# Kernel optimization log

Hardware: AMD Instinct MI355X
Metric: run time of the kernel (lower is better)

Reference implementation:

```python
import jax, jax.numpy as jnp
import numpy as np

DIM = 512
HEADS = 16
WS = 8          # window size
SHIFT = 4       # shift size
POSMLP = 32
MLP_HID = 4 * DIM
B = 32
HH = 56
WW = 56
EPS = 1e-5


def setup_inputs() -> dict:
    key = jax.random.key(0)
    ks = jax.random.split(key, 20)
    s = 0.02
    inp = {
        'x': jax.random.normal(ks[0], (B, HH * WW, DIM), jnp.float32),
        'g1': jnp.ones((DIM,), jnp.float32),
        'be1': jnp.zeros((DIM,), jnp.float32),
        'w_qkv': s * jax.random.normal(ks[1], (3 * DIM, DIM), jnp.float32),
        'b_qkv': jnp.zeros((3 * DIM,), jnp.float32),
        'pm_w1': s * jax.random.normal(ks[2], (POSMLP, 2), jnp.float32),
        'pm_b1': jnp.zeros((POSMLP,), jnp.float32),
        'pm_w2': s * jax.random.normal(ks[3], (HEADS, POSMLP), jnp.float32),
        'pm_b2': jnp.zeros((HEADS,), jnp.float32),
        'w_proj': s * jax.random.normal(ks[4], (DIM, DIM), jnp.float32),
        'b_proj': jnp.zeros((DIM,), jnp.float32),
        'g2': jnp.ones((DIM,), jnp.float32),
        'be2': jnp.zeros((DIM,), jnp.float32),
        'w_fc1': s * jax.random.normal(ks[5], (MLP_HID, DIM), jnp.float32),
        'b_fc1': jnp.zeros((MLP_HID,), jnp.float32),
        'w_fc2': s * jax.random.normal(ks[6], (DIM, MLP_HID), jnp.float32),
        'b_fc2': jnp.zeros((DIM,), jnp.float32),
        'H': HH,
        'W': WW,
    }
    return inp


def _layernorm(x, g, b):
    m = jnp.mean(x, -1, keepdims=True)
    v = jnp.mean(jnp.square(x - m), -1, keepdims=True)
    return (x - m) * jax.lax.rsqrt(v + EPS) * g + b


def _shift_mask(H, W, ws, sh):
    # static numpy construction of the (nW, N, N) 0/-100 shift mask
    img = np.zeros((H, W), np.float32)
    cnt = 0
    for hs in (slice(0, -ws), slice(-ws, -sh), slice(-sh, None)):
        for wsl in (slice(0, -ws), slice(-ws, -sh), slice(-sh, None)):
            img[hs, wsl] = cnt
            cnt += 1
    mw = img.reshape(H // ws, ws, W // ws, ws).transpose(0, 2, 1, 3).reshape(-1, ws * ws)
    diff = mw[:, None, :] - mw[:, :, None]
    return jnp.asarray(np.where(diff != 0, -100.0, 0.0).astype(np.float32))


def _pos_bias(ws, pm_w1, pm_b1, pm_w2, pm_b2):
    # log-CPB relative position bias computed by a tiny MLP -> (heads, N, N)
    g = jnp.stack(jnp.meshgrid(jnp.arange(ws), jnp.arange(ws), indexing='ij'))
    coords = g.reshape(2, -1).astype(jnp.float32)        # [2, N]
    d = coords[:, :, None] - coords[:, None, :]          # [2, N, N]
    d = jnp.sign(d) * jnp.log1p(jnp.abs(d))
    h = jax.nn.relu(jnp.einsum('cnm,oc->onm', d, pm_w1) + pm_b1[:, None, None])
    return jnp.einsum('onm,ho->hnm', h, pm_w2) + pm_b2[:, None, None]


def reference(x, g1, be1, w_qkv, b_qkv, pm_w1, pm_b1, pm_w2, pm_b2,
              w_proj, b_proj, g2, be2, w_fc1, b_fc1, w_fc2, b_fc2, H, W):
    ws, sh, nh = WS, SHIFT, HEADS
    Bb, L, C = x.shape
    hd = C // nh
    scale = hd ** -0.5
    N = ws * ws
    nWh, nWw = H // ws, W // ws
    nW = nWh * nWw

    shortcut = x
    xn = _layernorm(x, g1, be1).reshape(Bb, H, W, C)
    xn = jnp.roll(xn, (-sh, -sh), axis=(1, 2))
    # window partition -> (B*nW, N, C)
    xw = xn.reshape(Bb, nWh, ws, nWw, ws, C).transpose(0, 1, 3, 2, 4, 5).reshape(-1, N, C)

    qkv = (xw @ w_qkv.T + b_qkv).reshape(-1, N, 3, nh, hd).transpose(2, 0, 3, 1, 4)
    q, k, v = qkv[0], qkv[1], qkv[2]           # each (B*nW, nh, N, hd)

    attn = jnp.einsum('bhnd,bhmd->bhnm', q * scale, k)
    attn = attn + _pos_bias(ws, pm_w1, pm_b1, pm_w2, pm_b2)[None]

    mask = _shift_mask(H, W, ws, sh)           # (nW, N, N)
    attn = attn.reshape(Bb, nW, nh, N, N) + mask[None, :, None]
    attn = jax.nn.softmax(attn.reshape(-1, nh, N, N), axis=-1)

    out = jnp.einsum('bhnm,bhmd->bhnd', attn, v).transpose(0, 2, 1, 3).reshape(-1, N, C)
    out = out @ w_proj.T + b_proj

    # window reverse + roll back
    out = out.reshape(Bb, nWh, nWw, ws, ws, C).transpose(0, 1, 3, 2, 4, 5).reshape(Bb, H, W, C)
    out = jnp.roll(out, (sh, sh), axis=(1, 2)).reshape(Bb, L, C)

    x1 = shortcut + out
    h = jax.nn.gelu(_layernorm(x1, g2, be2) @ w_fc1.T + b_fc1, approximate=False)
    return x1 + (h @ w_fc2.T + b_fc2)
```

## Files before the change

### kernel.cpp

```cpp
#include <hip/hip_runtime.h>
#include <math.h>

typedef __bf16 bf16;
typedef bf16 bf16x8 __attribute__((ext_vector_type(8)));
typedef float f32x4 __attribute__((ext_vector_type(4)));

#define MFMA_BF16(a, b, c) __builtin_amdgcn_mfma_f32_16x16x32_bf16((a), (b), (c), 0, 0, 0)
#define GLDS16(gp, lp)                                                            \
  __builtin_amdgcn_global_load_lds((__attribute__((address_space(1))) void*)(gp), \
                                   (__attribute__((address_space(3))) void*)(lp), 16, 0, 0)

static constexpr int kDim   = 512;
static constexpr int kHeads = 16;
static constexpr int kHd    = 32;
static constexpr int kNt    = 64;
static constexpr int kNw    = 49;
static constexpr int kL     = 3136;
static constexpr int kToks  = 100352;
static constexpr int kWins  = 1568;
static constexpr int kHid   = 2048;
static constexpr size_t kQS = (size_t)kWins * kHeads * kNt * kHd;

__global__ __launch_bounds__(256) void wconv_kernel(const float* __restrict__ s,
                                                    bf16* __restrict__ d, int n8) {
  int i = blockIdx.x * 256 + threadIdx.x;
  if (i >= n8) return;
  const float4 a = *(const float4*)(s + i * 8);
  const float4 b = *(const float4*)(s + i * 8 + 4);
  bf16x8 o;
  o[0] = (bf16)a.x; o[1] = (bf16)a.y; o[2] = (bf16)a.z; o[3] = (bf16)a.w;
  o[4] = (bf16)b.x; o[5] = (bf16)b.y; o[6] = (bf16)b.z; o[7] = (bf16)b.w;
  *(bf16x8*)(d + i * 8) = o;
}

__global__ void posbias_kernel(const float* __restrict__ w1, const float* __restrict__ b1,
                               const float* __restrict__ w2, const float* __restrict__ b2,
                               float* __restrict__ tbl) {
  int idx = blockIdx.x * 256 + threadIdx.x;
  if (idx >= kHeads * kNt * kNt) return;
  int h = idx >> 12, n = (idx >> 6) & 63, m = idx & 63;
  float dr = (float)((n >> 3) - (m >> 3));
  float dc = (float)((n & 7) - (m & 7));
  dr = (dr > 0.f ? 1.f : (dr < 0.f ? -1.f : 0.f)) * log1pf(fabsf(dr));
  dc = (dc > 0.f ? 1.f : (dc < 0.f ? -1.f : 0.f)) * log1pf(fabsf(dc));
  float acc = b2[h];
  for (int o = 0; o < 32; ++o) {
    float hv = w1[o * 2] * dr + w1[o * 2 + 1] * dc + b1[o];
    acc += w2[h * 32 + o] * fmaxf(hv, 0.f);
  }
  tbl[idx] = acc;
}

template <int MODE>
__global__ __launch_bounds__(256) void ln_kernel(const float* __restrict__ x,
                                                 const float* __restrict__ g,
                                                 const float* __restrict__ be,
                                                 bf16* __restrict__ o) {
  const int t = blockIdx.x * 4 + (threadIdx.x >> 6);
  const int lane = threadIdx.x & 63;
  size_t src;
  if (MODE == 0) {
    const int win = t >> 6, n = t & 63;
    const int b = win / kNw, wi = win % kNw;
    const int h0 = ((wi / 7) * 8 + (n >> 3) + 4) % 56;
    const int w0 = ((wi % 7) * 8 + (n & 7) + 4) % 56;
    src = ((size_t)b * kL + h0 * 56 + w0) * kDim;
  } else {
    src = (size_t)t * kDim;
  }
  const float4 a = *(const float4*)(x + src + lane * 8);
  const float4 bq = *(const float4*)(x + src + lane * 8 + 4);
  float xf[8] = {a.x, a.y, a.z, a.w, bq.x, bq.y, bq.z, bq.w};
  float s = 0.f, s2 = 0.f;
#pragma unroll
  for (int j = 0; j < 8; ++j) { s += xf[j]; s2 += xf[j] * xf[j]; }
#pragma unroll
  for (int off = 32; off > 0; off >>= 1) { s += __shfl_xor(s, off); s2 += __shfl_xor(s2, off); }
  const float mean = s * (1.f / 512.f);
  const float rstd = rsqrtf(s2 * (1.f / 512.f) - mean * mean + 1e-5f);
  const float4 ga = *(const float4*)(g + lane * 8);
  const float4 gb = *(const float4*)(g + lane * 8 + 4);
  const float4 ba = *(const float4*)(be + lane * 8);
  const float4 bb = *(const float4*)(be + lane * 8 + 4);
  const float gv[8] = {ga.x, ga.y, ga.z, ga.w, gb.x, gb.y, gb.z, gb.w};
  const float bv[8] = {ba.x, ba.y, ba.z, ba.w, bb.x, bb.y, bb.z, bb.w};
  bf16x8 ov;
#pragma unroll
  for (int j = 0; j < 8; ++j) ov[j] = (bf16)((xf[j] - mean) * rstd * gv[j] + bv[j]);
  *(bf16x8*)(o + (size_t)t * kDim + lane * 8) = ov;
}

template <int EPI>
__global__ __launch_bounds__(256) void gemm_bt(const bf16* __restrict__ A, const bf16* __restrict__ B,
                                               const float* __restrict__ bias, void* __restrict__ Cv,
                                               const float* __restrict__ extra, int N, int K) {
  __shared__ bf16 lA[128 * 64];
  __shared__ bf16 lB[128 * 64];
  const int nbn = N >> 7;
  const int bm = (int)blockIdx.x / nbn, bn = (int)blockIdx.x % nbn;
  const int tid = threadIdx.x;
  const int wave = tid >> 6, lane = tid & 63;
  const int wm = (wave >> 1) * 64, wn = (wave & 1) * 64;
  const int quad = lane >> 4, l16 = lane & 15;
  const int m7 = l16 & 7;
  f32x4 acc[4][4] = {};
  const int rloc = tid >> 3;
  const int csw = ((tid & 7) ^ (rloc & 7)) * 8;
  const bf16* pa = A + (size_t)(bm * 128 + rloc) * K + csw;
  const bf16* pb = B + (size_t)(bn * 128 + rloc) * K + csw;
  for (int kt = 0; kt < K; kt += 64) {
#pragma unroll
    for (int i = 0; i < 4; ++i) GLDS16(pa + (size_t)i * 32 * K + kt, lA + i * 2048 + tid * 8);
#pragma unroll
    for (int i = 0; i < 4; ++i) GLDS16(pb + (size_t)i * 32 * K + kt, lB + i * 2048 + tid * 8);
    __syncthreads();
#pragma unroll
    for (int kk = 0; kk < 2; ++kk) {
      const int pc = ((kk * 4 + quad) ^ m7) * 8;
      bf16x8 af[4], bfr[4];
#pragma unroll
      for (int mi = 0; mi < 4; ++mi)
        af[mi] = *(const bf16x8*)(lA + (wm + mi * 16 + l16) * 64 + pc);
#pragma unroll
      for (int ni = 0; ni < 4; ++ni)
        bfr[ni] = *(const bf16x8*)(lB + (wn + ni * 16 + l16) * 64 + pc);
#pragma unroll
      for (int mi = 0; mi < 4; ++mi)
#pragma unroll
        for (int ni = 0; ni < 4; ++ni) acc[mi][ni] = MFMA_BF16(af[mi], bfr[ni], acc[mi][ni]);
    }
    __syncthreads();
  }
  bf16* Cb = (bf16*)Cv;
  float* Cf = (float*)Cv;
#pragma unroll
  for (int mi = 0; mi < 4; ++mi) {
#pragma unroll
    for (int ni = 0; ni < 4; ++ni) {
      const int col = bn * 128 + wn + ni * 16 + l16;
      const float bb = bias[col];
#pragma unroll
      for (int r = 0; r < 4; ++r) {
        const int row = bm * 128 + wm + mi * 16 + quad * 4 + r;
        float val = acc[mi][ni][r] + bb;
        if constexpr (EPI == 1) {
          const int which = col >> 9, head = (col >> 5) & 15, d = col & 31;
          const int win = row >> 6, n = row & 63;
          Cb[(size_t)which * kQS + (((size_t)win * kHeads + head) * kNt + n) * kHd + d] = (bf16)val;
        } else if constexpr (EPI == 2) {
          val = 0.5f * val * (1.f + erff(val * 0.70710678118654752f));
          Cb[(size_t)row * N + col] = (bf16)val;
        } else if constexpr (EPI == 3) {
          Cf[(size_t)row * N + col] = val + extra[(size_t)row * N + col];
        } else {
          const int win = row >> 6, n = row & 63;
          const int b = win / kNw, wi = win % kNw;
          const int h0 = ((wi / 7) * 8 + (n >> 3) + 4) % 56;
          const int w0 = ((wi % 7) * 8 + (n & 7) + 4) % 56;
          const size_t dst = ((size_t)b * kL + h0 * 56 + w0) * kDim + col;
          Cf[dst] = val + extra[dst];
        }
      }
    }
  }
}

__device__ __forceinline__ int reg3(int x) { return x < 48 ? 0 : (x < 52 ? 1 : 2); }

__global__ __launch_bounds__(128) void attn_kernel(const bf16* __restrict__ qkv,
                                                   const float* __restrict__ ptbl,
                                                   bf16* __restrict__ out) {
  __shared__ float Sb[2][64 * 65];
  __shared__ float Rs[2][64];
  __shared__ bf16  Pb[2][64 * 72];
  __shared__ bf16  Vt[2][32 * 72];
  const int w = threadIdx.x >> 6, lane = threadIdx.x & 63;
  const int gwh = blockIdx.x * 2 + w;
  const int win = gwh >> 4, h = gwh & 15;
  const int quad = lane >> 4, l16 = lane & 15;
  const bf16* q = qkv + ((size_t)win * kHeads + h) * (kNt * kHd);
  const bf16* k = q + kQS;
  const bf16* v = q + 2 * kQS;

#pragma unroll
  for (int i = 0; i < 4; ++i) {
    const int row = i * 16 + (lane >> 2);
    const int d0 = (lane & 3) * 8;
    bf16x8 vv = *(const bf16x8*)(v + row * kHd + d0);
#pragma unroll
    for (int j = 0; j < 8; ++j) Vt[w][(d0 + j) * 72 + row] = vv[j];
  }

  bf16x8 qf[4], kf[4];
#pragma unroll
  for (int i = 0; i < 4; ++i) qf[i] = *(const bf16x8*)(q + (i * 16 + l16) * kHd + quad * 8);
#pragma unroll
  for (int j = 0; j < 4; ++j) kf[j] = *(const bf16x8*)(k + (j * 16 + l16) * kHd + quad * 8);
  f32x4 sa[4][4] = {};
#pragma unroll
  for (int i = 0; i < 4; ++i)
#pragma unroll
    for (int j = 0; j < 4; ++j) sa[i][j] = MFMA_BF16(qf[i], kf[j], sa[i][j]);

  const int wi = win % kNw;
  const int hb = (wi / 7) * 8, wb = (wi % 7) * 8;
  const float* bh = ptbl + h * 4096;
#pragma unroll
  for (int i = 0; i < 4; ++i) {
#pragma unroll
    for (int j = 0; j < 4; ++j) {
      const int ct = j * 16 + l16;
      const int crg = reg3(hb + (ct >> 3)) * 3 + reg3(wb + (ct & 7));
#pragma unroll
      for (int r = 0; r < 4; ++r) {
        const int rt = i * 16 + quad * 4 + r;
        const int rrg = reg3(hb + (rt >> 3)) * 3 + reg3(wb + (rt & 7));
        float sv = sa[i][j][r] * 0.17677669529663687f + bh[rt * 64 + ct];
        if (rrg != crg) sv -= 100.f;
        Sb[w][rt * 65 + ct] = sv;
      }
    }
  }
  __syncthreads();

  float mx = -1e30f;
  for (int i = 0; i < 64; ++i) mx = fmaxf(mx, Sb[w][lane * 65 + i]);
  float sum = 0.f;
  for (int i = 0; i < 64; ++i) {
    const float p = __expf(Sb[w][lane * 65 + i] - mx);
    sum += p;
    Pb[w][lane * 72 + i] = (bf16)p;
  }
  Rs[w][lane] = 1.f / sum;
  __syncthreads();

  f32x4 oa[4][2] = {};
#pragma unroll
  for (int kk = 0; kk < 2; ++kk) {
    bf16x8 pf[4], vf[2];
#pragma unroll
    for (int mi = 0; mi < 4; ++mi)
      pf[mi] = *(const bf16x8*)(&Pb[w][(mi * 16 + l16) * 72 + kk * 32 + quad * 8]);
#pragma unroll
    for (int nj = 0; nj < 2; ++nj)
      vf[nj] = *(const bf16x8*)(&Vt[w][(nj * 16 + l16) * 72 + kk * 32 + quad * 8]);
#pragma unroll
    for (int mi = 0; mi < 4; ++mi)
#pragma unroll
      for (int nj = 0; nj < 2; ++nj) oa[mi][nj] = MFMA_BF16(pf[mi], vf[nj], oa[mi][nj]);
  }
#pragma unroll
  for (int mi = 0; mi < 4; ++mi)
#pragma unroll
    for (int nj = 0; nj < 2; ++nj)
#pragma unroll
      for (int r = 0; r < 4; ++r) {
        const int row = mi * 16 + quad * 4 + r;
        const int col = nj * 16 + l16;
        out[((size_t)win * kNt + row) * kDim + h * kHd + col] = (bf16)(oa[mi][nj][r] * Rs[w][row]);
      }
}

extern "C" void kernel_launch(void* const* d_in, const int* in_sizes, int n_in,
                              void* d_out, int out_size, void* d_ws, size_t ws_size,
                              hipStream_t stream) {
  (void)in_sizes; (void)n_in; (void)out_size; (void)ws_size;
  const float* x      = (const float*)d_in[0];
  const float* g1     = (const float*)d_in[1];
  const float* be1    = (const float*)d_in[2];
  const float* w_qkv  = (const float*)d_in[3];
  const float* b_qkv  = (const float*)d_in[4];
  const float* pm_w1  = (const float*)d_in[5];
  const float* pm_b1  = (const float*)d_in[6];
  const float* pm_w2  = (const float*)d_in[7];
  const float* pm_b2  = (const float*)d_in[8];
  const float* w_proj = (const float*)d_in[9];
  const float* b_proj = (const float*)d_in[10];
  const float* g2     = (const float*)d_in[11];
  const float* be2    = (const float*)d_in[12];
  const float* w_fc1  = (const float*)d_in[13];
  const float* b_fc1  = (const float*)d_in[14];
  const float* w_fc2  = (const float*)d_in[15];
  const float* b_fc2  = (const float*)d_in[16];
  float* out = (float*)d_out;
  char* ws = (char*)d_ws;

  constexpr size_t OFF_WB   = 1u << 20;
  constexpr size_t OFF_XW   = OFF_WB + (8u << 20);
  constexpr size_t SZ_ACT   = (size_t)kToks * kDim * 2;
  constexpr size_t OFF_QKV  = OFF_XW + SZ_ACT;
  float* biastbl = (float*)ws;
  bf16* wqb = (bf16*)(ws + OFF_WB);
  bf16* wpb = wqb + 786432;
  bf16* w1b = wpb + 262144;
  bf16* w2b = w1b + 1048576;
  bf16* xw    = (bf16*)(ws + OFF_XW);
  bf16* attnb = xw;
  bf16* xn2   = xw;
  bf16* qkvb = (bf16*)(ws + OFF_QKV);
  float* x1  = (float*)(ws + OFF_QKV);
  bf16* hbuf = (bf16*)(ws + OFF_QKV + (size_t)kToks * kDim * 4);

  wconv_kernel<<<dim3(786432 / 2048), dim3(256), 0, stream>>>(w_qkv, wqb, 786432 / 8);
  wconv_kernel<<<dim3(262144 / 2048), dim3(256), 0, stream>>>(w_proj, wpb, 262144 / 8);
  wconv_kernel<<<dim3(1048576 / 2048), dim3(256), 0, stream>>>(w_fc1, w1b, 1048576 / 8);
  wconv_kernel<<<dim3(1048576 / 2048), dim3(256), 0, stream>>>(w_fc2, w2b, 1048576 / 8);
  posbias_kernel<<<dim3(256), dim3(256), 0, stream>>>(pm_w1, pm_b1, pm_w2, pm_b2, biastbl);
  ln_kernel<0><<<dim3(kToks / 4), dim3(256), 0, stream>>>(x, g1, be1, xw);
  gemm_bt<1><<<dim3((kToks / 128) * (1536 / 128)), dim3(256), 0, stream>>>(
      xw, wqb, b_qkv, qkvb, nullptr, 1536, 512);
  attn_kernel<<<dim3(kWins * kHeads / 2), dim3(128), 0, stream>>>(qkvb, biastbl, attnb);
  gemm_bt<4><<<dim3((kToks / 128) * (512 / 128)), dim3(256), 0, stream>>>(
      attnb, wpb, b_proj, x1, x, 512, 512);
  ln_kernel<1><<<dim3(kToks / 4), dim3(256), 0, stream>>>(x1, g2, be2, xn2);
  constexpr int kChunk = kToks / 4;
  for (int c = 0; c < 4; ++c) {
    const size_t ro = (size_t)c * kChunk * kDim;
    gemm_bt<2><<<dim3((kChunk / 128) * (kHid / 128)), dim3(256), 0, stream>>>(
        xn2 + ro, w1b, b_fc1, hbuf, nullptr, kHid, 512);
    gemm_bt<3><<<dim3((kChunk / 128) * (512 / 128)), dim3(256), 0, stream>>>(
        hbuf, w2b, b_fc2, out + ro, x1 + ro, 512, kHid);
  }
}
```

Baseline: 1.810 ms.

## Replace 128x128 GEMM with double-buffered 256x256 tile, 8-wave pipelined kernel

Swaps the simple 128x128 single-buffered GEMM for a 256x256 tile kernel with 512 threads and double-buffered LDS. Next-tile global-to-LDS loads are interleaved with MFMA phases using explicit vmcnt waits, barriers and setprio. It also remaps workgroup IDs across the XCDs for locality and uses a new swizzled LDS layout. The aim is to hide load latency and raise arithmetic intensity, at the cost of heavy register use (one block per CU) and fewer workgroups per launch.

```diff
diff --git a/kernel.cpp b/kernel.cpp
--- a/kernel.cpp
+++ b/kernel.cpp
@@ -9,6 +9,10 @@
 #define GLDS16(gp, lp)                                                            \
   __builtin_amdgcn_global_load_lds((__attribute__((address_space(1))) void*)(gp), \
                                    (__attribute__((address_space(3))) void*)(lp), 16, 0, 0)
+#define VMCNT4 asm volatile("s_waitcnt vmcnt(4)" ::: "memory")
+#define LGKM0 asm volatile("s_waitcnt lgkmcnt(0)" ::: "memory")
+#define SBAR __builtin_amdgcn_s_barrier()
+#define SCHED0 __builtin_amdgcn_sched_barrier(0)
 
 static constexpr int kDim   = 512;
 static constexpr int kHeads = 16;
@@ -90,58 +94,114 @@
   *(bf16x8*)(o + (size_t)t * kDim + lane * 8) = ov;
 }
 
+#define READ_A(KH, MB)                                             \
+  _Pragma("unroll") for (int i = 0; i < 4; ++i)                    \
+      af[i] = *(const bf16x8*)(&L[cb][0][KH][aoff + (MB + i) * 512]);
+#define READ_B(KH)                                                 \
+  _Pragma("unroll") for (int i = 0; i < 4; ++i)                    \
+      bfr[i] = *(const bf16x8*)(&L[cb][1][KH][boff + i * 512]);
+#define MFMAS(MB)                                                  \
+  LGKM0;                                                           \
+  SCHED0;                                                          \
+  __builtin_amdgcn_s_setprio(1);                                   \
+  _Pragma("unroll") for (int mi = 0; mi < 4; ++mi)                 \
+  _Pragma("unroll") for (int ni = 0; ni < 4; ++ni)                 \
+      acc[MB + mi][ni] = MFMA_BF16(af[mi], bfr[ni], acc[MB + mi][ni]); \
+  __builtin_amdgcn_s_setprio(0)
+
 template <int EPI>
-__global__ __launch_bounds__(256) void gemm_bt(const bf16* __restrict__ A, const bf16* __restrict__ B,
-                                               const float* __restrict__ bias, void* __restrict__ Cv,
-                                               const float* __restrict__ extra, int N, int K) {
-  __shared__ bf16 lA[128 * 64];
-  __shared__ bf16 lB[128 * 64];
-  const int nbn = N >> 7;
-  const int bm = (int)blockIdx.x / nbn, bn = (int)blockIdx.x % nbn;
-  const int tid = threadIdx.x;
+__global__ __launch_bounds__(512, 1) void gemm256(const bf16* __restrict__ A, const bf16* __restrict__ B,
+                                                  const float* __restrict__ bias, void* __restrict__ Cv,
+                                                  const float* __restrict__ extra, int N, int K) {
+  __shared__ __align__(16) bf16 L[2][2][2][8192];
+  const int nbn = N >> 8;
+  const int nwg = (int)gridDim.x;
+  int wg = (int)blockIdx.x;
+  {
+    const int q = nwg >> 3, r = nwg & 7;
+    const int xcd = wg & 7, loc = wg >> 3;
+    wg = (xcd < r ? xcd * (q + 1) : r * (q + 1) + (xcd - r) * q) + loc;
+  }
+  const int bm = wg / nbn, bn = wg % nbn;
+  const int tid = (int)threadIdx.x;
   const int wave = tid >> 6, lane = tid & 63;
-  const int wm = (wave >> 1) * 64, wn = (wave & 1) * 64;
+  const int wm2 = wave >> 2, wn4 = wave & 3;
   const int quad = lane >> 4, l16 = lane & 15;
-  const int m7 = l16 & 7;
-  f32x4 acc[4][4] = {};
-  const int rloc = tid >> 3;
-  const int csw = ((tid & 7) ^ (rloc & 7)) * 8;
-  const bf16* pa = A + (size_t)(bm * 128 + rloc) * K + csw;
-  const bf16* pb = B + (size_t)(bn * 128 + rloc) * K + csw;
+
+  const int sl0 = tid, sl1 = 512 + tid;
+  const int rp0 = sl0 >> 3, ls0 = (sl0 & 7) ^ (rp0 & 7);
+  const int rp1 = sl1 >> 3, ls1 = (sl1 & 7) ^ (rp1 & 7);
+  const int row0 = rp0 * 2 + (ls0 >> 2), c0 = ls0 & 3;
+  const int row1 = rp1 * 2 + (ls1 >> 2), c1 = ls1 & 3;
+  const bf16* pa0 = A + (size_t)(bm * 256 + row0) * K + c0 * 8;
+  const bf16* pa1 = A + (size_t)(bm * 256 + row1) * K + c1 * 8;
+  const bf16* pb0 = B + (size_t)(bn * 256 + row0) * K + c0 * 8;
+  const bf16* pb1 = B + (size_t)(bn * 256 + row1) * K + c1 * 8;
+
+  const int ar = wm2 * 128 + l16, arp = ar >> 1;
+  const int aoff = (arp * 8 + ((((ar & 1) << 2) | quad) ^ (arp & 7))) * 8;
+  const int br = wn4 * 64 + l16, brp = br >> 1;
+  const int boff = (brp * 8 + ((((br & 1) << 2) | quad) ^ (brp & 7))) * 8;
+
+  f32x4 acc[8][4] = {};
+  bf16x8 af[4], bfr[4];
+
+  GLDS16(pa0, &L[0][0][0][sl0 * 8]);
+  GLDS16(pa1, &L[0][0][0][sl1 * 8]);
+  GLDS16(pb0, &L[0][1][0][sl0 * 8]);
+  GLDS16(pb1, &L[0][1][0][sl1 * 8]);
+  GLDS16(pa0 + 32, &L[0][0][1][sl0 * 8]);
+  GLDS16(pa1 + 32, &L[0][0][1][sl1 * 8]);
+  GLDS16(pb0 + 32, &L[0][1][1][sl0 * 8]);
+  GLDS16(pb1 + 32, &L[0][1][1][sl1 * 8]);
+  VMCNT4;
+  SBAR;
+
+#pragma unroll 2
   for (int kt = 0; kt < K; kt += 64) {
-#pragma unroll
-    for (int i = 0; i < 4; ++i) GLDS16(pa + (size_t)i * 32 * K + kt, lA + i * 2048 + tid * 8);
-#pragma unroll
-    for (int i = 0; i < 4; ++i) GLDS16(pb + (size_t)i * 32 * K + kt, lB + i * 2048 + tid * 8);
-    __syncthreads();
-#pragma unroll
-    for (int kk = 0; kk < 2; ++kk) {
-      const int pc = ((kk * 4 + quad) ^ m7) * 8;
-      bf16x8 af[4], bfr[4];
-#pragma unroll
-      for (int mi = 0; mi < 4; ++mi)
-        af[mi] = *(const bf16x8*)(lA + (wm + mi * 16 + l16) * 64 + pc);
-#pragma unroll
-      for (int ni = 0; ni < 4; ++ni)
-        bfr[ni] = *(const bf16x8*)(lB + (wn + ni * 16 + l16) * 64 + pc);
-#pragma unroll
-      for (int mi = 0; mi < 4; ++mi)
-#pragma unroll
-        for (int ni = 0; ni < 4; ++ni) acc[mi][ni] = MFMA_BF16(af[mi], bfr[ni], acc[mi][ni]);
-    }
-    __syncthreads();
-  }
+    const int cb = (kt >> 6) & 1, nb = cb ^ 1;
+    const int kn = (kt + 64 < K) ? (kt + 64) : kt;
+    READ_A(0, 0);
+    READ_B(0);
+    GLDS16(pa0 + kn, &L[nb][0][0][sl0 * 8]);
+    GLDS16(pa1 + kn, &L[nb][0][0][sl1 * 8]);
+    SBAR;
+    MFMAS(0);
+    SBAR;
+    READ_A(0, 4);
+    GLDS16(pb0 + kn, &L[nb][1][0][sl0 * 8]);
+    GLDS16(pb1 + kn, &L[nb][1][0][sl1 * 8]);
+    SBAR;
+    MFMAS(4);
+    VMCNT4;
+    SBAR;
+    READ_A(1, 0);
+    READ_B(1);
+    GLDS16(pa0 + kn + 32, &L[nb][0][1][sl0 * 8]);
+    GLDS16(pa1 + kn + 32, &L[nb][0][1][sl1 * 8]);
+    SBAR;
+    MFMAS(0);
+    SBAR;
+    READ_A(1, 4);
+    GLDS16(pb0 + kn + 32, &L[nb][1][1][sl0 * 8]);
+    GLDS16(pb1 + kn + 32, &L[nb][1][1][sl1 * 8]);
+    SBAR;
+    MFMAS(4);
+    VMCNT4;
+    SBAR;
+  }
+
   bf16* Cb = (bf16*)Cv;
   float* Cf = (float*)Cv;
 #pragma unroll
-  for (int mi = 0; mi < 4; ++mi) {
+  for (int mi = 0; mi < 8; ++mi) {
 #pragma unroll
     for (int ni = 0; ni < 4; ++ni) {
-      const int col = bn * 128 + wn + ni * 16 + l16;
+      const int col = bn * 256 + wn4 * 64 + ni * 16 + l16;
       const float bb = bias[col];
 #pragma unroll
       for (int r = 0; r < 4; ++r) {
-        const int row = bm * 128 + wm + mi * 16 + quad * 4 + r;
+        const int row = bm * 256 + wm2 * 128 + mi * 16 + quad * 4 + r;
         float val = acc[mi][ni][r] + bb;
         if constexpr (EPI == 1) {
           const int which = col >> 9, head = (col >> 5) & 15, d = col & 31;
@@ -307,18 +367,18 @@
   wconv_kernel<<<dim3(1048576 / 2048), dim3(256), 0, stream>>>(w_fc2, w2b, 1048576 / 8);
   posbias_kernel<<<dim3(256), dim3(256), 0, stream>>>(pm_w1, pm_b1, pm_w2, pm_b2, biastbl);
   ln_kernel<0><<<dim3(kToks / 4), dim3(256), 0, stream>>>(x, g1, be1, xw);
-  gemm_bt<1><<<dim3((kToks / 128) * (1536 / 128)), dim3(256), 0, stream>>>(
+  gemm256<1><<<dim3((kToks / 256) * (1536 / 256)), dim3(512), 0, stream>>>(
       xw, wqb, b_qkv, qkvb, nullptr, 1536, 512);
   attn_kernel<<<dim3(kWins * kHeads / 2), dim3(128), 0, stream>>>(qkvb, biastbl, attnb);
-  gemm_bt<4><<<dim3((kToks / 128) * (512 / 128)), dim3(256), 0, stream>>>(
+  gemm256<4><<<dim3((kToks / 256) * (512 / 256)), dim3(512), 0, stream>>>(
       attnb, wpb, b_proj, x1, x, 512, 512);
   ln_kernel<1><<<dim3(kToks / 4), dim3(256), 0, stream>>>(x1, g2, be2, xn2);
   constexpr int kChunk = kToks / 4;
   for (int c = 0; c < 4; ++c) {
     const size_t ro = (size_t)c * kChunk * kDim;
-    gemm_bt<2><<<dim3((kChunk / 128) * (kHid / 128)), dim3(256), 0, stream>>>(
+    gemm256<2><<<dim3((kChunk / 256) * (kHid / 256)), dim3(512), 0, stream>>>(
         xn2 + ro, w1b, b_fc1, hbuf, nullptr, kHid, 512);
-    gemm_bt<3><<<dim3((kChunk / 128) * (512 / 128)), dim3(256), 0, stream>>>(
+    gemm256<3><<<dim3((kChunk / 256) * (512 / 256)), dim3(512), 0, stream>>>(
         hbuf, w2b, b_fc2, out + ro, x1 + ro, 512, kHid);
   }
 }
```

Measured after the change: 1.660 ms. 1.09x faster.
